# Kernel tuning notes

Measured on AMD Instinct MI355X. Metric: run time of the kernel, lower is better.

## Reference

```python
import jax, jax.numpy as jnp
import numpy as np

EMB = 1024
HEADS = 16
HEAD_DIM = EMB // HEADS
B, S = 4, 2048


def setup_inputs() -> dict:
    key = jax.random.key(0)
    ks = jax.random.split(key, 7)
    sc = 1.0 / np.sqrt(EMB)
    return {
        "query": jax.random.normal(ks[0], (B, S, EMB), jnp.float32),
        "key": jax.random.normal(ks[1], (B, S, EMB), jnp.float32),
        "value": jax.random.normal(ks[2], (B, S, EMB), jnp.float32),
        "Wq": jax.random.normal(ks[3], (EMB, EMB), jnp.float32) * sc,
        "Wk": jax.random.normal(ks[4], (EMB, EMB), jnp.float32) * sc,
        "Wv": jax.random.normal(ks[5], (EMB, EMB), jnp.float32) * sc,
        "Wo": jax.random.normal(ks[6], (EMB, EMB), jnp.float32) * sc,
    }


def reference(query, key, value, Wq, Wk, Wv, Wo):
    # nn.Linear applies x @ W^T; W stored as [out, in]
    def split_heads(x):  # [B,S,E] -> [B,H,S,D]
        return x.reshape(B, -1, HEADS, HEAD_DIM).transpose(0, 2, 1, 3)

    q = split_heads(query @ Wq.T)
    k = split_heads(key @ Wk.T)
    v = split_heads(value @ Wv.T)
    scores = jnp.einsum('bhse,bhte->bhst', q, k) / np.sqrt(HEAD_DIM).astype(np.float32)
    attn = jax.nn.softmax(scores, axis=-1)
    ctx = jnp.einsum('bhst,bhtd->bshd', attn, v)  # [B,S,H,D]
    out = ctx.reshape(B, -1, EMB) @ Wo.T
    return out
```

## Files before the change

kernel.cpp:

```cpp
#include <hip/hip_runtime.h>
#include <hip/hip_bf16.h>

#define EMB   1024
#define HEADS 16
#define HDIM  64
#define BB    4
#define SS    2048
#define MROWS (BB*SS)

typedef __bf16 bf16_t;
typedef __bf16 bf16x4_t __attribute__((ext_vector_type(4)));
typedef __bf16 bf16x8   __attribute__((ext_vector_type(8)));
typedef float  f32x4    __attribute__((ext_vector_type(4)));

__device__ __forceinline__ void glds16(const void* g, void* l) {
  __builtin_amdgcn_global_load_lds(
      (const __attribute__((address_space(1))) void*)g,
      (__attribute__((address_space(3))) void*)l, 16, 0, 0);
}

__launch_bounds__(256)
__global__ void cast_w(const float* s0, const float* s1, const float* s2,
                       const float* s3,
                       bf16_t* d0, bf16_t* d1, bf16_t* d2, bf16_t* d3) {
  const int z = blockIdx.z;
  const float* ss[4] = {s0, s1, s2, s3};
  bf16_t*      dd[4] = {d0, d1, d2, d3};
  const float* s = ss[z];
  bf16_t*      d = dd[z];
  const int i = (blockIdx.x*256 + threadIdx.x) * 8;
  const f32x4 a = *(const f32x4*)&s[i];
  const f32x4 b = *(const f32x4*)&s[i+4];
  bf16x8 r;
  r[0]=(bf16_t)a[0]; r[1]=(bf16_t)a[1]; r[2]=(bf16_t)a[2]; r[3]=(bf16_t)a[3];
  r[4]=(bf16_t)b[0]; r[5]=(bf16_t)b[1]; r[6]=(bf16_t)b[2]; r[7]=(bf16_t)b[3];
  *(bf16x8*)&d[i] = r;
}

__launch_bounds__(256)
__global__ void gemm_qkv(const float* A0, const float* A1, const float* A2,
                         const bf16_t* W0, const bf16_t* W1, const bf16_t* W2,
                         bf16_t* C0, bf16_t* C1, bf16_t* C2, float sscale) {
  __shared__ __align__(16) float  Asf[4096];
  __shared__ __align__(16) bf16_t Bs[4096];
  const int tid  = threadIdx.x;
  const int wave = tid >> 6, lane = tid & 63;
  const int quad = lane >> 4, l16 = lane & 15;
  const int wm = wave >> 1, wn = wave & 1;

  const int fid = blockIdx.x + 8*(blockIdx.y + 64*blockIdx.z);
  const int xcd = fid & 7, s = fid >> 3;
  const int bn0 = (s & 7) * 128;
  const int p   = xcd + 8*(s >> 3);
  const int z   = p >> 6;
  const int bm0 = (p & 63) * 128;

  const float*  A = (z == 0) ? A0 : (z == 1) ? A1 : A2;
  const bf16_t* W = (z == 0) ? W0 : (z == 1) ? W1 : W2;
  bf16_t*       C = (z == 0) ? C0 : (z == 1) ? C1 : C2;
  const float oscale = (z == 0) ? sscale : 1.0f;

  const int arow = lane >> 3;
  const int aslt = (lane & 7) ^ arow;
  f32x4 acc[4][4] = {};

  for (int k0 = 0; k0 < EMB; k0 += 32) {
#pragma unroll
    for (int c = 0; c < 4; ++c) {
      const int i = wave*4 + c;
      glds16(A + (size_t)(bm0 + i*8 + arow)*EMB + k0 + aslt*4,
             &Asf[i*256]);
    }
#pragma unroll
    for (int j = 0; j < 2; ++j) {
      const int i   = wave*2 + j;
      const int row = i*16 + (lane >> 2);
      const int col = (lane & 3) * 8;
      glds16(W + (size_t)(bn0 + row)*EMB + k0 + col, &Bs[i*512]);
    }
    __syncthreads();

    bf16x8 a[4], b[4];
#pragma unroll
    for (int t2 = 0; t2 < 4; ++t2) {
      const int rl = wm*64 + t2*16 + l16;
      const float* Ab = &Asf[(rl >> 3)*256 + (rl & 7)*32];
      const f32x4 v0 = *(const f32x4*)&Ab[(((quad*2)    ) ^ (rl & 7))*4];
      const f32x4 v1 = *(const f32x4*)&Ab[(((quad*2) + 1) ^ (rl & 7))*4];
#pragma unroll
      for (int r = 0; r < 4; ++r) {
        a[t2][r]     = (bf16_t)v0[r];
        a[t2][4 + r] = (bf16_t)v1[r];
      }
      b[t2] = *(const bf16x8*)&Bs[(wn*64 + t2*16 + l16)*32 + quad*8];
    }
#pragma unroll
    for (int mt = 0; mt < 4; ++mt)
#pragma unroll
      for (int nt = 0; nt < 4; ++nt)
        acc[mt][nt] = __builtin_amdgcn_mfma_f32_16x16x32_bf16(a[mt], b[nt], acc[mt][nt], 0, 0, 0);
    __syncthreads();
  }

  if (z == 2) {
    const int bb = bm0 >> 11;
    const int T  = ((bm0 & 2047) >> 6) + wm;
    const int h  = (bn0 >> 6) + wn;
    bf16_t* base = C + ((size_t)(bb*HEADS + h)*32 + T)*4096;
#pragma unroll
    for (int ks = 0; ks < 2; ++ks)
#pragma unroll
      for (int nt = 0; nt < 4; ++nt) {
        bf16x8 v;
#pragma unroll
        for (int r = 0; r < 4; ++r) {
          v[r]     = (bf16_t)acc[2*ks][nt][r];
          v[4 + r] = (bf16_t)acc[2*ks + 1][nt][r];
        }
        *(bf16x8*)&base[((nt*2 + ks)*64 + quad*16 + l16)*8] = v;
      }
  } else {
#pragma unroll
    for (int mt = 0; mt < 4; ++mt) {
      const int row = bm0 + wm*64 + mt*16 + quad*4;
#pragma unroll
      for (int nt = 0; nt < 4; ++nt) {
        const int col = bn0 + wn*64 + nt*16 + l16;
#pragma unroll
        for (int r = 0; r < 4; ++r)
          C[(size_t)(row + r)*EMB + col] = (bf16_t)(acc[mt][nt][r] * oscale);
      }
    }
  }
}

__device__ __forceinline__ void gemm_core(const bf16_t* __restrict__ A,
                                          const bf16_t* __restrict__ W,
                                          bf16_t* As, bf16_t* Bs,
                                          f32x4 acc[4][4],
                                          int bm0, int bn0,
                                          int wave, int lane) {
  const int quad = lane >> 4, l16 = lane & 15;
  const int wm = wave >> 1, wn = wave & 1;
  for (int k0 = 0; k0 < EMB; k0 += 32) {
#pragma unroll
    for (int j = 0; j < 2; ++j) {
      const int i   = wave*2 + j;
      const int row = i*16 + (lane >> 2);
      const int col = (lane & 3) * 8;
      glds16(A + (size_t)(bm0 + row)*EMB + k0 + col, &As[i*512]);
      glds16(W + (size_t)(bn0 + row)*EMB + k0 + col, &Bs[i*512]);
    }
    __syncthreads();

    bf16x8 a[4], b[4];
#pragma unroll
    for (int t = 0; t < 4; ++t) {
      a[t] = *(const bf16x8*)&As[(wm*64 + t*16 + l16)*32 + quad*8];
      b[t] = *(const bf16x8*)&Bs[(wn*64 + t*16 + l16)*32 + quad*8];
    }
#pragma unroll
    for (int mt = 0; mt < 4; ++mt)
#pragma unroll
      for (int nt = 0; nt < 4; ++nt)
        acc[mt][nt] = __builtin_amdgcn_mfma_f32_16x16x32_bf16(a[mt], b[nt], acc[mt][nt], 0, 0, 0);
    __syncthreads();
  }
}

__launch_bounds__(256)
__global__ void gemm_out(const bf16_t* __restrict__ A, const bf16_t* __restrict__ W,
                         float* __restrict__ C) {
  __shared__ __align__(16) bf16_t As[128*32];
  __shared__ __align__(16) bf16_t Bs[128*32];
  const int tid  = threadIdx.x;
  const int wave = tid >> 6, lane = tid & 63;
  const int quad = lane >> 4, l16 = lane & 15;
  const int wm = wave >> 1, wn = wave & 1;

  const int fid = blockIdx.x + 8*blockIdx.y;
  const int xcd = fid & 7, s = fid >> 3;
  const int bn0 = (s & 7) * 128;
  const int bm0 = (xcd*8 + (s >> 3)) * 128;

  f32x4 acc[4][4] = {};
  gemm_core(A, W, As, Bs, acc, bm0, bn0, wave, lane);

#pragma unroll
  for (int mt = 0; mt < 4; ++mt) {
    const int row = bm0 + wm*64 + mt*16 + quad*4;
#pragma unroll
    for (int nt = 0; nt < 4; ++nt) {
      const int col = bn0 + wn*64 + nt*16 + l16;
#pragma unroll
      for (int r = 0; r < 4; ++r)
        C[(size_t)(row + r)*EMB + col] = acc[mt][nt][r];
    }
  }
}

__launch_bounds__(512, 8)
__global__ void attn(const bf16_t* Qp, const bf16_t* __restrict__ Kp,
                     const bf16_t* __restrict__ Vt, bf16_t* Cx) {
  __shared__ __align__(16) bf16_t Ks[2][4096];
  __shared__ __align__(16) bf16_t Vs[2][4096];

  const int tid  = threadIdx.x;
  const int wave = tid >> 6, lane = tid & 63;
  const int quad = lane >> 4, l16 = lane & 15;

  const int fid  = blockIdx.x + 16*(blockIdx.y + 16*blockIdx.z);
  const int xcd  = fid & 7, s = fid >> 3;
  const int q0   = (s & 15) * 128;
  const int pair = xcd*8 + (s >> 4);
  const int h    = pair & 15;
  const int b    = pair >> 4;

  bf16x8 qf[2];
  {
    const size_t qr = (size_t)(b*SS + q0 + wave*16 + l16)*EMB + h*HDIM;
    qf[0] = *(const bf16x8*)&Qp[qr + quad*8];
    qf[1] = *(const bf16x8*)&Qp[qr + 32 + quad*8];
  }

  const bf16_t* Kb = Kp + (size_t)b*SS*EMB + h*HDIM;
  const bf16_t* Vb = Vt + ((size_t)(b*HEADS + h)*32)*4096;

  f32x4 o[4] = {};
  f32x4 lsv = {};

  auto stage = [&](int ti, int bf) {
    const int t0 = ti * 64;
    const int i  = wave;
    glds16(Kb + (size_t)(t0 + (i&3)*16 + l16)*EMB + (i>>2)*32 + quad*8,
           &Ks[bf][i*512]);
    glds16(Vb + (size_t)ti*4096 + i*512 + lane*8, &Vs[bf][i*512]);
  };

  stage(0, 0);

  const int NT = SS / 64;
  for (int t = 0, buf = 0; t < NT; ++t, buf ^= 1) {
    __syncthreads();
    if (t + 1 < NT) stage(t + 1, buf ^ 1);

    f32x4 st[4] = {};
#pragma unroll
    for (int cb = 0; cb < 4; ++cb) {
      const bf16x8 kf0 = *(const bf16x8*)&Ks[buf][cb*512 + lane*8];
      const bf16x8 kf1 = *(const bf16x8*)&Ks[buf][2048 + cb*512 + lane*8];
      st[cb] = __builtin_amdgcn_mfma_f32_16x16x32_bf16(kf0, qf[0], st[cb], 0, 0, 0);
      st[cb] = __builtin_amdgcn_mfma_f32_16x16x32_bf16(kf1, qf[1], st[cb], 0, 0, 0);
    }

#pragma unroll
    for (int kb = 0; kb < 4; ++kb) {
#pragma unroll
      for (int r = 0; r < 4; ++r)
        st[kb][r] = __builtin_amdgcn_exp2f(st[kb][r]);
      lsv += st[kb];
    }
    bf16x8 pb[2];
#pragma unroll
    for (int ks = 0; ks < 2; ++ks)
#pragma unroll
      for (int r = 0; r < 4; ++r) {
        pb[ks][r]     = (bf16_t)st[2*ks][r];
        pb[ks][4 + r] = (bf16_t)st[2*ks + 1][r];
      }

#pragma unroll
    for (int ks = 0; ks < 2; ++ks)
#pragma unroll
      for (int dt = 0; dt < 4; ++dt) {
        const bf16x8 vf = *(const bf16x8*)&Vs[buf][((dt*2 + ks)*64 + lane)*8];
        o[dt] = __builtin_amdgcn_mfma_f32_16x16x32_bf16(vf, pb[ks], o[dt], 0, 0, 0);
      }
  }

  float l = lsv[0] + lsv[1] + lsv[2] + lsv[3];
  l += __shfl_xor(l, 16, 64);
  l += __shfl_xor(l, 32, 64);
  const float inv = 1.0f / l;
  const size_t row = (size_t)(b*SS + q0 + wave*16 + l16)*EMB + h*HDIM;
#pragma unroll
  for (int dt = 0; dt < 4; ++dt) {
    bf16x4_t v;
#pragma unroll
    for (int r = 0; r < 4; ++r) v[r] = (bf16_t)(o[dt][r] * inv);
    *(bf16x4_t*)&Cx[row + dt*16 + quad*4] = v;
  }
}

extern "C" void kernel_launch(void* const* d_in, const int* in_sizes, int n_in,
                              void* d_out, int out_size, void* d_ws, size_t ws_size,
                              hipStream_t stream) {
  (void)in_sizes; (void)n_in; (void)out_size; (void)ws_size;
  const float* query = (const float*)d_in[0];
  const float* key   = (const float*)d_in[1];
  const float* value = (const float*)d_in[2];
  const float* WqF   = (const float*)d_in[3];
  const float* WkF   = (const float*)d_in[4];
  const float* WvF   = (const float*)d_in[5];
  const float* WoF   = (const float*)d_in[6];

  const size_t AN = (size_t)MROWS*EMB;
  const size_t WN = (size_t)EMB*EMB;
  float* out = (float*)d_out;
  bf16_t* S5 = (bf16_t*)d_out;
  bf16_t* S6 = S5 + AN;

  bf16_t* S2  = (bf16_t*)d_ws;
  bf16_t* Wqb = S2 + AN;
  bf16_t* Wkb = Wqb + WN;
  bf16_t* Wvb = Wkb + WN;
  bf16_t* Wob = Wvb + WN;

  const float sscale = 0.125f * 1.44269504f;

  const dim3 gw  (512, 1, 4);
  const dim3 gqkv(EMB/128, MROWS/128, 3);
  const dim3 gg  (EMB/128, MROWS/128);
  const dim3 gattn(SS/128, HEADS, BB);

  cast_w<<<gw, 256, 0, stream>>>(WqF, WkF, WvF, WoF, Wqb, Wkb, Wvb, Wob);
  gemm_qkv<<<gqkv, 256, 0, stream>>>(query, key, value, Wqb, Wkb, Wvb,
                                     S2, S6, S5, sscale);
  attn<<<gattn, 512, 0, stream>>>(S2, S6, S5, S2);
  gemm_out<<<gg, 256, 0, stream>>>(S2, Wob, out);
}
```

Baseline: 344.1 us.

## Shrink output GEMM M-tile to 64 and re-layout QKV fp32 A-tile in LDS

The output projection GEMM now uses 64x128 tiles instead of 128x128, doubling the block count from 512 to 1024 to improve CU occupancy and load balance, at the cost of less reuse of W per block. Separately, the QKV GEMM's fp32 A-tile LDS layout changes from an XOR-swizzled row layout to a fragment-ordered one, where each lane writes and reads its own contiguous 16 bytes. This is meant to make LDS reads conflict-free without swizzle index math. The shared gemm_core helper is removed and inlined into gemm_out.

```diff
diff --git a/kernel.cpp b/kernel.cpp
--- a/kernel.cpp
+++ b/kernel.cpp
@@ -41,8 +41,8 @@
 __global__ void gemm_qkv(const float* A0, const float* A1, const float* A2,
                          const bf16_t* W0, const bf16_t* W1, const bf16_t* W2,
                          bf16_t* C0, bf16_t* C1, bf16_t* C2, float sscale) {
-  __shared__ __align__(16) float  Asf[4096];
-  __shared__ __align__(16) bf16_t Bs[4096];
+  __shared__ __align__(16) float  Asf[16*256];
+  __shared__ __align__(16) bf16_t Bs[8*512];
   const int tid  = threadIdx.x;
   const int wave = tid >> 6, lane = tid & 63;
   const int quad = lane >> 4, l16 = lane & 15;
@@ -60,16 +60,15 @@
   bf16_t*       C = (z == 0) ? C0 : (z == 1) ? C1 : C2;
   const float oscale = (z == 0) ? sscale : 1.0f;
 
-  const int arow = lane >> 3;
-  const int aslt = (lane & 7) ^ arow;
   f32x4 acc[4][4] = {};
 
   for (int k0 = 0; k0 < EMB; k0 += 32) {
 #pragma unroll
-    for (int c = 0; c < 4; ++c) {
-      const int i = wave*4 + c;
-      glds16(A + (size_t)(bm0 + i*8 + arow)*EMB + k0 + aslt*4,
-             &Asf[i*256]);
+    for (int cc = 0; cc < 4; ++cc) {
+      const int c = wave*4 + cc;
+      const int g = c >> 1, h = c & 1;
+      glds16(A + (size_t)(bm0 + g*16 + l16)*EMB + k0 + quad*8 + h*4,
+             &Asf[c*256]);
     }
 #pragma unroll
     for (int j = 0; j < 2; ++j) {
@@ -83,10 +82,9 @@
     bf16x8 a[4], b[4];
 #pragma unroll
     for (int t2 = 0; t2 < 4; ++t2) {
-      const int rl = wm*64 + t2*16 + l16;
-      const float* Ab = &Asf[(rl >> 3)*256 + (rl & 7)*32];
-      const f32x4 v0 = *(const f32x4*)&Ab[(((quad*2)    ) ^ (rl & 7))*4];
-      const f32x4 v1 = *(const f32x4*)&Ab[(((quad*2) + 1) ^ (rl & 7))*4];
+      const int g = wm*4 + t2;
+      const f32x4 v0 = *(const f32x4*)&Asf[(g*2    )*256 + lane*4];
+      const f32x4 v1 = *(const f32x4*)&Asf[(g*2 + 1)*256 + lane*4];
 #pragma unroll
       for (int r = 0; r < 4; ++r) {
         a[t2][r]     = (bf16_t)v0[r];
@@ -134,44 +132,10 @@
   }
 }
 
-__device__ __forceinline__ void gemm_core(const bf16_t* __restrict__ A,
-                                          const bf16_t* __restrict__ W,
-                                          bf16_t* As, bf16_t* Bs,
-                                          f32x4 acc[4][4],
-                                          int bm0, int bn0,
-                                          int wave, int lane) {
-  const int quad = lane >> 4, l16 = lane & 15;
-  const int wm = wave >> 1, wn = wave & 1;
-  for (int k0 = 0; k0 < EMB; k0 += 32) {
-#pragma unroll
-    for (int j = 0; j < 2; ++j) {
-      const int i   = wave*2 + j;
-      const int row = i*16 + (lane >> 2);
-      const int col = (lane & 3) * 8;
-      glds16(A + (size_t)(bm0 + row)*EMB + k0 + col, &As[i*512]);
-      glds16(W + (size_t)(bn0 + row)*EMB + k0 + col, &Bs[i*512]);
-    }
-    __syncthreads();
-
-    bf16x8 a[4], b[4];
-#pragma unroll
-    for (int t = 0; t < 4; ++t) {
-      a[t] = *(const bf16x8*)&As[(wm*64 + t*16 + l16)*32 + quad*8];
-      b[t] = *(const bf16x8*)&Bs[(wn*64 + t*16 + l16)*32 + quad*8];
-    }
-#pragma unroll
-    for (int mt = 0; mt < 4; ++mt)
-#pragma unroll
-      for (int nt = 0; nt < 4; ++nt)
-        acc[mt][nt] = __builtin_amdgcn_mfma_f32_16x16x32_bf16(a[mt], b[nt], acc[mt][nt], 0, 0, 0);
-    __syncthreads();
-  }
-}
-
 __launch_bounds__(256)
 __global__ void gemm_out(const bf16_t* __restrict__ A, const bf16_t* __restrict__ W,
                          float* __restrict__ C) {
-  __shared__ __align__(16) bf16_t As[128*32];
+  __shared__ __align__(16) bf16_t As[64*32];
   __shared__ __align__(16) bf16_t Bs[128*32];
   const int tid  = threadIdx.x;
   const int wave = tid >> 6, lane = tid & 63;
@@ -181,14 +145,44 @@
   const int fid = blockIdx.x + 8*blockIdx.y;
   const int xcd = fid & 7, s = fid >> 3;
   const int bn0 = (s & 7) * 128;
-  const int bm0 = (xcd*8 + (s >> 3)) * 128;
-
-  f32x4 acc[4][4] = {};
-  gemm_core(A, W, As, Bs, acc, bm0, bn0, wave, lane);
-
-#pragma unroll
-  for (int mt = 0; mt < 4; ++mt) {
-    const int row = bm0 + wm*64 + mt*16 + quad*4;
+  const int bm0 = (xcd*16 + (s >> 3)) * 64;
+
+  f32x4 acc[2][4] = {};
+
+  for (int k0 = 0; k0 < EMB; k0 += 32) {
+    {
+      const int i   = wave;
+      const int row = i*16 + (lane >> 2);
+      const int col = (lane & 3) * 8;
+      glds16(A + (size_t)(bm0 + row)*EMB + k0 + col, &As[i*512]);
+    }
+#pragma unroll
+    for (int j = 0; j < 2; ++j) {
+      const int i   = wave*2 + j;
+      const int row = i*16 + (lane >> 2);
+      const int col = (lane & 3) * 8;
+      glds16(W + (size_t)(bn0 + row)*EMB + k0 + col, &Bs[i*512]);
+    }
+    __syncthreads();
+
+    bf16x8 a[2], b[4];
+#pragma unroll
+    for (int t2 = 0; t2 < 2; ++t2)
+      a[t2] = *(const bf16x8*)&As[(wm*32 + t2*16 + l16)*32 + quad*8];
+#pragma unroll
+    for (int t2 = 0; t2 < 4; ++t2)
+      b[t2] = *(const bf16x8*)&Bs[(wn*64 + t2*16 + l16)*32 + quad*8];
+#pragma unroll
+    for (int mt = 0; mt < 2; ++mt)
+#pragma unroll
+      for (int nt = 0; nt < 4; ++nt)
+        acc[mt][nt] = __builtin_amdgcn_mfma_f32_16x16x32_bf16(a[mt], b[nt], acc[mt][nt], 0, 0, 0);
+    __syncthreads();
+  }
+
+#pragma unroll
+  for (int mt = 0; mt < 2; ++mt) {
+    const int row = bm0 + wm*32 + mt*16 + quad*4;
 #pragma unroll
     for (int nt = 0; nt < 4; ++nt) {
       const int col = bn0 + wn*64 + nt*16 + l16;
@@ -320,7 +314,7 @@
 
   const dim3 gw  (512, 1, 4);
   const dim3 gqkv(EMB/128, MROWS/128, 3);
-  const dim3 gg  (EMB/128, MROWS/128);
+  const dim3 gg  (8, 128);
   const dim3 gattn(SS/128, HEADS, BB);
 
   cast_w<<<gw, 256, 0, stream>>>(WqF, WkF, WvF, WoF, Wqb, Wkb, Wvb, Wob);
```

After: 379.1 us. +10.2%, slower.
